# Kernel tuning notes

Measured on AMD Instinct MI355X. Metric: run time of the kernel, lower is better.

Reference implementation:

```python
import jax, jax.numpy as jnp
import numpy as np

LOWERSIZE = 40


def setup_inputs() -> dict:
    key = jax.random.key(0)
    ks = jax.random.split(key, 6)
    N, x_dim, y_dim = 2048, 768, 768
    return {
        "x_samples": jax.random.normal(ks[0], (N, x_dim), dtype=jnp.float32),
        "y_samples": jax.random.normal(ks[1], (N, y_dim), dtype=jnp.float32),
        "W1": jax.random.normal(ks[2], (LOWERSIZE, x_dim + y_dim), dtype=jnp.float32) * 0.02,
        "b1": jax.random.normal(ks[3], (LOWERSIZE,), dtype=jnp.float32) * 0.02,
        "W2": jax.random.normal(ks[4], (1, LOWERSIZE), dtype=jnp.float32) * 0.02,
        "b2": jax.random.normal(ks[5], (1,), dtype=jnp.float32) * 0.02,
    }


def reference(x_samples, y_samples, W1, b1, W2, b2):
    # F(z) = W2 @ relu(W1 @ z + b1) + b2, z = cat(x, y)
    N = y_samples.shape[0]
    x_dim = x_samples.shape[1]
    W1x = W1[:, :x_dim]   # [40, x_dim]
    W1y = W1[:, x_dim:]   # [40, y_dim]

    # Diagonal term T0: F(cat(x_i, y_i)) -> [N, 1]
    h0 = jax.nn.relu(x_samples @ W1x.T + y_samples @ W1y.T + b1)
    T0 = h0 @ W2.T + b2

    # Pairwise term: T1[i, j] = F(cat(x_j, y_i)) - 1.
    # Split the first Linear over x and y to avoid materializing the
    # [N, N, x_dim+y_dim] concatenation (same math, linearity of W1).
    hx = x_samples @ W1x.T  # [N, 40]
    hy = y_samples @ W1y.T  # [N, 40]
    h = jax.nn.relu(hy[:, None, :] + hx[None, :, :] + b1)  # [N, N, 40]
    T1 = (h @ W2.T + b2 - 1.0)[..., 0]  # [N, N]

    lse = jax.nn.logsumexp(T1, axis=1) - jnp.log(jnp.float32(N))  # [N]
    lower_bound = T0.mean() - jnp.exp(lse).mean()
    return lower_bound
```

## Files before the change

kernel.cpp:

```cpp
#include <hip/hip_runtime.h>

#define NROWS 2048
#define KDIM  768
#define L     40
#define HN    (NROWS * L)

__global__ __launch_bounds__(256) void k_proj(const float* __restrict__ x,
                                              const float* __restrict__ y,
                                              const float* __restrict__ W1,
                                              const float* __restrict__ b1,
                                              float* __restrict__ hxb,
                                              float* __restrict__ hy) {
    const int which = blockIdx.y;
    const int oh    = blockIdx.z;
    const float* __restrict__ A = which ? y : x;
    const int tid = threadIdx.x;
    const int r   = tid >> 5;
    const int seg = tid & 31;
    const int row0 = blockIdx.x * 8;

    __shared__ float sh2[8 * 21];

    const float* arow = A + (size_t)(row0 + r) * KDIM;
    float4 a[6];
#pragma unroll
    for (int q = 0; q < 6; ++q)
        a[q] = *(const float4*)(arow + q * 128 + seg * 4);

    const float* wbase = W1 + (size_t)which * KDIM + (size_t)(oh * 20) * (2 * KDIM);
#pragma unroll 2
    for (int ol = 0; ol < 20; ++ol) {
        const float* wrow = wbase + (size_t)ol * (2 * KDIM);
        float s = 0.f;
#pragma unroll
        for (int q = 0; q < 6; ++q) {
            float4 w = *(const float4*)(wrow + q * 128 + seg * 4);
            s += a[q].x * w.x + a[q].y * w.y + a[q].z * w.z + a[q].w * w.w;
        }
        s += __shfl_xor(s, 16);
        s += __shfl_xor(s, 8);
        s += __shfl_xor(s, 4);
        s += __shfl_xor(s, 2);
        s += __shfl_xor(s, 1);
        if (seg == 0) sh2[r * 21 + ol] = s;
    }
    __syncthreads();

    if (tid < 8 * 20) {
        int rr = tid / 20, ol = tid - rr * 20;
        float s = sh2[rr * 21 + ol];
        int o = oh * 20 + ol;
        if (!which) {
            s += b1[o];
            hxb[(size_t)(row0 + rr) * L + o] = s;
        } else {
            hy[(size_t)(row0 + rr) * L + o] = s;
        }
    }
}

#define BI 128
#define BJ 64
#define STRD 44

__global__ __launch_bounds__(512, 4) void k_pair(const float* __restrict__ hxb,
                                                 const float* __restrict__ hy,
                                                 const float* __restrict__ W2,
                                                 const float* __restrict__ b2p,
                                                 float* __restrict__ pairE,
                                                 float* __restrict__ pairT) {
    __shared__ float shy[BI * STRD];
    __shared__ float shx[BJ * STRD];
    __shared__ float sw2[STRD];
    __shared__ float red[16];

    const int tid = threadIdx.x;
    const int i0 = blockIdx.x * BI;
    const int j0 = blockIdx.y * BJ;

    for (int idx = tid; idx < BI * 10; idx += 512) {
        int rr = idx / 10, c = idx - rr * 10;
        float4 v = ((const float4*)(hy + (size_t)i0 * L))[idx];
        *(float4*)(shy + rr * STRD + c * 4) = v;
    }
    for (int idx = tid; idx < BJ * 10; idx += 512) {
        int rr = idx / 10, c = idx - rr * 10;
        float4 v = ((const float4*)(hxb + (size_t)j0 * L))[idx];
        *(float4*)(shx + rr * STRD + c * 4) = v;
    }
    if (tid < 10) ((float4*)sw2)[tid] = ((const float4*)W2)[tid];
    __syncthreads();

    const int tx = tid & 15, ty = tid >> 4;

    float acc[4][4];
#pragma unroll
    for (int u = 0; u < 4; ++u)
#pragma unroll
        for (int v = 0; v < 4; ++v) acc[u][v] = 0.f;

    float4 ayA[4], axA[4], wA4;
    float4 ayB[4], axB[4], wB4;

#define LOADF(AY, AX, W4, K4) do {                                          \
    W4 = *(const float4*)(sw2 + (K4) * 4);                                  \
    _Pragma("unroll") for (int u_ = 0; u_ < 4; ++u_)                        \
        AY[u_] = *(const float4*)(shy + (ty + 32 * u_) * STRD + (K4) * 4);  \
    _Pragma("unroll") for (int v_ = 0; v_ < 4; ++v_)                        \
        AX[v_] = *(const float4*)(shx + (tx + 16 * v_) * STRD + (K4) * 4);  \
} while (0)

#define FMAF(AY, AX, W4) do {                                               \
    _Pragma("unroll") for (int u_ = 0; u_ < 4; ++u_)                        \
    _Pragma("unroll") for (int v_ = 0; v_ < 4; ++v_) {                      \
        float t;                                                            \
        t = AY[u_].x + AX[v_].x; t = fmaxf(t, 0.f); acc[u_][v_] += t * W4.x;\
        t = AY[u_].y + AX[v_].y; t = fmaxf(t, 0.f); acc[u_][v_] += t * W4.y;\
        t = AY[u_].z + AX[v_].z; t = fmaxf(t, 0.f); acc[u_][v_] += t * W4.z;\
        t = AY[u_].w + AX[v_].w; t = fmaxf(t, 0.f); acc[u_][v_] += t * W4.w;\
    }                                                                       \
} while (0)

    LOADF(ayA, axA, wA4, 0);
    LOADF(ayB, axB, wB4, 1);
    FMAF(ayA, axA, wA4); LOADF(ayA, axA, wA4, 2);
    FMAF(ayB, axB, wB4); LOADF(ayB, axB, wB4, 3);
    FMAF(ayA, axA, wA4); LOADF(ayA, axA, wA4, 4);
    FMAF(ayB, axB, wB4); LOADF(ayB, axB, wB4, 5);
    FMAF(ayA, axA, wA4); LOADF(ayA, axA, wA4, 6);
    FMAF(ayB, axB, wB4); LOADF(ayB, axB, wB4, 7);
    FMAF(ayA, axA, wA4); LOADF(ayA, axA, wA4, 8);
    FMAF(ayB, axB, wB4); LOADF(ayB, axB, wB4, 9);
    FMAF(ayA, axA, wA4);
    FMAF(ayB, axB, wB4);

#undef LOADF
#undef FMAF

    const float b2v = b2p[0];
    const float c1  = b2v - 1.f;
    float sumE = 0.f, sumT = 0.f;
#pragma unroll
    for (int u = 0; u < 4; ++u)
#pragma unroll
        for (int v = 0; v < 4; ++v) {
            int gi = i0 + ty + 32 * u;
            int gj = j0 + tx + 16 * v;
            float val = acc[u][v];
            if (gi == gj) sumT += val + b2v;
            sumE += __expf(val + c1);
        }

#pragma unroll
    for (int off = 32; off > 0; off >>= 1) {
        sumE += __shfl_down(sumE, off);
        sumT += __shfl_down(sumT, off);
    }
    int wid = tid >> 6;
    if ((tid & 63) == 0) { red[wid] = sumE; red[8 + wid] = sumT; }
    __syncthreads();
    if (tid == 0) {
        float e = 0.f, t = 0.f;
#pragma unroll
        for (int q = 0; q < 8; ++q) { e += red[q]; t += red[8 + q]; }
        int bid = blockIdx.y * gridDim.x + blockIdx.x;
        pairE[bid] = e;
        pairT[bid] = t;
    }
}

__global__ __launch_bounds__(512) void k_fin(const float* __restrict__ pairE,
                                             const float* __restrict__ pairT,
                                             float* __restrict__ out) {
    __shared__ float red[16];
    const int tid = threadIdx.x;
    float e = pairE[tid];
    float t = pairT[tid];
#pragma unroll
    for (int off = 32; off > 0; off >>= 1) {
        e += __shfl_down(e, off);
        t += __shfl_down(t, off);
    }
    int wid = tid >> 6;
    if ((tid & 63) == 0) { red[wid] = e; red[8 + wid] = t; }
    __syncthreads();
    if (tid == 0) {
        float se = 0.f, st = 0.f;
#pragma unroll
        for (int q = 0; q < 8; ++q) { se += red[q]; st += red[8 + q]; }
        const float invN = 1.0f / (float)NROWS;
        out[0] = st * invN - se * invN * invN;
    }
}

extern "C" void kernel_launch(void* const* d_in, const int* in_sizes, int n_in,
                              void* d_out, int out_size, void* d_ws, size_t ws_size,
                              hipStream_t stream) {
    const float* x  = (const float*)d_in[0];
    const float* y  = (const float*)d_in[1];
    const float* W1 = (const float*)d_in[2];
    const float* b1 = (const float*)d_in[3];
    const float* W2 = (const float*)d_in[4];
    const float* b2 = (const float*)d_in[5];
    float* out = (float*)d_out;

    float* wsf   = (float*)d_ws;
    float* hxb   = wsf;
    float* hy    = hxb + HN;
    float* pairE = hy + HN;
    float* pairT = pairE + 512;

    k_proj<<<dim3(NROWS / 8, 2, 2), 256, 0, stream>>>(x, y, W1, b1, hxb, hy);
    k_pair<<<dim3(NROWS / BI, NROWS / BJ), 512, 0, stream>>>(hxb, hy, W2, b2, pairE, pairT);
    k_fin<<<1, 512, 0, stream>>>(pairE, pairT, out);
}
```

Baseline: 97.15 us.

## Restructure projection kernel to stage W1 slices in LDS with split-K threads

Rewrites k_proj so each block loads a 10-output slice of W1 into shared memory once and reuses it across 32 rows. Each thread handles one row and one 96-float K segment, double-buffering its activation loads, then reduces partial sums through LDS. The aim is to cut repeated global reads of W1 and the per-output wave shuffle reductions of the old design. In exchange, x and y are now read four times (once per output group), and the kernel uses more LDS and registers.

```diff
diff --git a/kernel.cpp b/kernel.cpp
--- a/kernel.cpp
+++ b/kernel.cpp
@@ -4,6 +4,10 @@
 #define KDIM  768
 #define L     40
 #define HN    (NROWS * L)
+
+#define OPB   10
+#define RPB   32
+#define WF4   192
 
 __global__ __launch_bounds__(256) void k_proj(const float* __restrict__ x,
                                               const float* __restrict__ y,
@@ -11,50 +15,73 @@
                                               const float* __restrict__ b1,
                                               float* __restrict__ hxb,
                                               float* __restrict__ hy) {
-    const int which = blockIdx.y;
-    const int oh    = blockIdx.z;
+    const int og    = blockIdx.y;
+    const int which = blockIdx.z;
     const float* __restrict__ A = which ? y : x;
     const int tid = threadIdx.x;
-    const int r   = tid >> 5;
-    const int seg = tid & 31;
-    const int row0 = blockIdx.x * 8;
-
-    __shared__ float sh2[8 * 21];
-
-    const float* arow = A + (size_t)(row0 + r) * KDIM;
-    float4 a[6];
-#pragma unroll
-    for (int q = 0; q < 6; ++q)
-        a[q] = *(const float4*)(arow + q * 128 + seg * 4);
-
-    const float* wbase = W1 + (size_t)which * KDIM + (size_t)(oh * 20) * (2 * KDIM);
-#pragma unroll 2
-    for (int ol = 0; ol < 20; ++ol) {
-        const float* wrow = wbase + (size_t)ol * (2 * KDIM);
-        float s = 0.f;
-#pragma unroll
-        for (int q = 0; q < 6; ++q) {
-            float4 w = *(const float4*)(wrow + q * 128 + seg * 4);
-            s += a[q].x * w.x + a[q].y * w.y + a[q].z * w.z + a[q].w * w.w;
-        }
-        s += __shfl_xor(s, 16);
-        s += __shfl_xor(s, 8);
-        s += __shfl_xor(s, 4);
-        s += __shfl_xor(s, 2);
-        s += __shfl_xor(s, 1);
-        if (seg == 0) sh2[r * 21 + ol] = s;
-    }
-    __syncthreads();
-
-    if (tid < 8 * 20) {
-        int rr = tid / 20, ol = tid - rr * 20;
-        float s = sh2[rr * 21 + ol];
-        int o = oh * 20 + ol;
+    const int r   = tid & 31;
+    const int s   = tid >> 5;
+    const int row0 = blockIdx.x * RPB;
+    const int o0   = og * OPB;
+
+    __shared__ float4 wlds[OPB * WF4];
+
+    const float4* W1f4 = (const float4*)W1;
+    for (int i = tid; i < OPB * WF4; i += 256) {
+        int ol = i / WF4, q = i - ol * WF4;
+        wlds[ol * WF4 + q] = W1f4[(size_t)(o0 + ol) * 384 + which * WF4 + q];
+    }
+
+    const float4* arow = (const float4*)(A + (size_t)(row0 + r) * KDIM) + s * 24;
+
+    float acc[OPB];
+#pragma unroll
+    for (int ol = 0; ol < OPB; ++ol) acc[ol] = 0.f;
+
+    float4 aA[8], aB[8];
+#pragma unroll
+    for (int j = 0; j < 8; ++j) aA[j] = arow[j];
+    __syncthreads();
+
+#define COMPUTE(AR, C) do {                                                  \
+    _Pragma("unroll") for (int ol = 0; ol < OPB; ++ol) {                     \
+        const float4* wp = &wlds[ol * WF4 + s * 24 + (C) * 8];               \
+        float sacc = 0.f;                                                    \
+        _Pragma("unroll") for (int j = 0; j < 8; ++j) {                      \
+            float4 w = wp[j];                                                \
+            sacc += AR[j].x * w.x + AR[j].y * w.y                            \
+                  + AR[j].z * w.z + AR[j].w * w.w;                           \
+        }                                                                    \
+        acc[ol] += sacc;                                                     \
+    } } while (0)
+
+#pragma unroll
+    for (int j = 0; j < 8; ++j) aB[j] = arow[8 + j];
+    COMPUTE(aA, 0);
+#pragma unroll
+    for (int j = 0; j < 8; ++j) aA[j] = arow[16 + j];
+    COMPUTE(aB, 1);
+    COMPUTE(aA, 2);
+#undef COMPUTE
+
+    __syncthreads();
+    float* red = (float*)wlds;
+#pragma unroll
+    for (int ol = 0; ol < OPB; ++ol)
+        red[(ol * 8 + s) * 32 + r] = acc[ol];
+    __syncthreads();
+
+    for (int idx = tid; idx < RPB * OPB; idx += 256) {
+        int rr = idx / OPB, ol = idx - rr * OPB;
+        float v = 0.f;
+#pragma unroll
+        for (int ss = 0; ss < 8; ++ss)
+            v += red[(ol * 8 + ss) * 32 + rr];
+        int o = o0 + ol;
         if (!which) {
-            s += b1[o];
-            hxb[(size_t)(row0 + rr) * L + o] = s;
+            hxb[(size_t)(row0 + rr) * L + o] = v + b1[o];
         } else {
-            hy[(size_t)(row0 + rr) * L + o] = s;
+            hy[(size_t)(row0 + rr) * L + o] = v;
         }
     }
 }
@@ -210,7 +237,7 @@
     float* pairE = hy + HN;
     float* pairT = pairE + 512;
 
-    k_proj<<<dim3(NROWS / 8, 2, 2), 256, 0, stream>>>(x, y, W1, b1, hxb, hy);
+    k_proj<<<dim3(NROWS / RPB, 4, 2), 256, 0, stream>>>(x, y, W1, b1, hxb, hy);
     k_pair<<<dim3(NROWS / BI, NROWS / BJ), 512, 0, stream>>>(hxb, hy, W2, b2, pairE, pairT);
     k_fin<<<1, 512, 0, stream>>>(pairE, pairT, out);
 }
```

Measured after the change: 95.85 us. About the same (-1.3%).

## Fuse projection and pairwise kernels with inter-block flag synchronization

Applied to the files above, without the earlier changes.

Merges the projection kernel into the pairwise kernel. Each of the 512 blocks first computes 4 rows of hx and 4 of hy, then publishes a per-block flag. Blocks spin-wait only on the specific producer blocks whose rows they need before loading tiles. This removes a kernel launch boundary and lets projection and pairwise work overlap, but it depends on all 512 blocks being co-resident to avoid deadlock. The flags use a magic value XOR the block id rather than being reset, so stale flags from an earlier call could satisfy the wait before the data is rewritten.

```diff
diff --git a/kernel.cpp b/kernel.cpp
--- a/kernel.cpp
+++ b/kernel.cpp
@@ -4,79 +4,78 @@
 #define KDIM  768
 #define L     40
 #define HN    (NROWS * L)
-
-__global__ __launch_bounds__(256) void k_proj(const float* __restrict__ x,
-                                              const float* __restrict__ y,
-                                              const float* __restrict__ W1,
-                                              const float* __restrict__ b1,
-                                              float* __restrict__ hxb,
-                                              float* __restrict__ hy) {
-    const int which = blockIdx.y;
-    const int oh    = blockIdx.z;
-    const float* __restrict__ A = which ? y : x;
-    const int tid = threadIdx.x;
-    const int r   = tid >> 5;
-    const int seg = tid & 31;
-    const int row0 = blockIdx.x * 8;
-
-    __shared__ float sh2[8 * 21];
-
-    const float* arow = A + (size_t)(row0 + r) * KDIM;
-    float4 a[6];
-#pragma unroll
-    for (int q = 0; q < 6; ++q)
-        a[q] = *(const float4*)(arow + q * 128 + seg * 4);
-
-    const float* wbase = W1 + (size_t)which * KDIM + (size_t)(oh * 20) * (2 * KDIM);
-#pragma unroll 2
-    for (int ol = 0; ol < 20; ++ol) {
-        const float* wrow = wbase + (size_t)ol * (2 * KDIM);
-        float s = 0.f;
-#pragma unroll
-        for (int q = 0; q < 6; ++q) {
-            float4 w = *(const float4*)(wrow + q * 128 + seg * 4);
-            s += a[q].x * w.x + a[q].y * w.y + a[q].z * w.z + a[q].w * w.w;
-        }
-        s += __shfl_xor(s, 16);
-        s += __shfl_xor(s, 8);
-        s += __shfl_xor(s, 4);
-        s += __shfl_xor(s, 2);
-        s += __shfl_xor(s, 1);
-        if (seg == 0) sh2[r * 21 + ol] = s;
-    }
-    __syncthreads();
-
-    if (tid < 8 * 20) {
-        int rr = tid / 20, ol = tid - rr * 20;
-        float s = sh2[rr * 21 + ol];
-        int o = oh * 20 + ol;
-        if (!which) {
-            s += b1[o];
-            hxb[(size_t)(row0 + rr) * L + o] = s;
-        } else {
-            hy[(size_t)(row0 + rr) * L + o] = s;
-        }
-    }
-}
+#define MAGICF 0x7A3F0000u
 
 #define BI 128
 #define BJ 64
 #define STRD 44
 
-__global__ __launch_bounds__(512, 4) void k_pair(const float* __restrict__ hxb,
-                                                 const float* __restrict__ hy,
-                                                 const float* __restrict__ W2,
-                                                 const float* __restrict__ b2p,
-                                                 float* __restrict__ pairE,
-                                                 float* __restrict__ pairT) {
+__global__ __launch_bounds__(512, 4) void k_fused(
+    const float* __restrict__ x, const float* __restrict__ y,
+    const float* __restrict__ W1, const float* __restrict__ b1,
+    const float* __restrict__ W2, const float* __restrict__ b2p,
+    float* __restrict__ hxb, float* __restrict__ hy,
+    unsigned* __restrict__ flags,
+    float* __restrict__ pairE, float* __restrict__ pairT)
+{
+    const int tid  = threadIdx.x;
+    const int b    = blockIdx.x;
+    const int wv   = tid >> 6;
+    const int lane = tid & 63;
+
+    {
+        const int which = wv >> 2;
+        const int row   = b * 4 + (wv & 3);
+        const float* A  = which ? y : x;
+        const float4* af = (const float4*)(A + (size_t)row * KDIM);
+        float4 a0 = af[lane], a1 = af[64 + lane], a2 = af[128 + lane];
+        const float4* wb = (const float4*)W1 + which * 192;
+        float keep = 0.f;
+#pragma unroll 4
+        for (int o = 0; o < L; ++o) {
+            const float4* wf = wb + (size_t)o * 384;
+            float4 w0 = wf[lane], w1 = wf[64 + lane], w2 = wf[128 + lane];
+            float s = a0.x*w0.x + a0.y*w0.y + a0.z*w0.z + a0.w*w0.w
+                    + a1.x*w1.x + a1.y*w1.y + a1.z*w1.z + a1.w*w1.w
+                    + a2.x*w2.x + a2.y*w2.y + a2.z*w2.z + a2.w*w2.w;
+            s += __shfl_xor(s, 32);
+            s += __shfl_xor(s, 16);
+            s += __shfl_xor(s, 8);
+            s += __shfl_xor(s, 4);
+            s += __shfl_xor(s, 2);
+            s += __shfl_xor(s, 1);
+            if (lane == o) keep = s;
+        }
+        if (lane < L) {
+            float v = keep;
+            if (!which) { v += b1[lane]; hxb[(size_t)row * L + lane] = v; }
+            else        {                hy [(size_t)row * L + lane] = v; }
+        }
+    }
+    __syncthreads();
+    if (tid == 0) {
+        __threadfence();
+        __hip_atomic_store(&flags[b], MAGICF ^ (unsigned)b,
+                           __ATOMIC_RELEASE, __HIP_MEMORY_SCOPE_AGENT);
+    }
+
+    const int bx = b & 15, by = b >> 4;
+    const int i0 = bx * BI, j0 = by * BJ;
+
+    if (tid < 48) {
+        int p = (tid < 32) ? (bx * 32 + tid) : (by * 16 + (tid - 32));
+        unsigned want = MAGICF ^ (unsigned)p;
+        while (__hip_atomic_load(&flags[p], __ATOMIC_RELAXED,
+                                 __HIP_MEMORY_SCOPE_AGENT) != want)
+            __builtin_amdgcn_s_sleep(2);
+        __threadfence();
+    }
+    __syncthreads();
+
     __shared__ float shy[BI * STRD];
     __shared__ float shx[BJ * STRD];
     __shared__ float sw2[STRD];
     __shared__ float red[16];
-
-    const int tid = threadIdx.x;
-    const int i0 = blockIdx.x * BI;
-    const int j0 = blockIdx.y * BJ;
 
     for (int idx = tid; idx < BI * 10; idx += 512) {
         int rr = idx / 10, c = idx - rr * 10;
@@ -163,9 +162,8 @@
         float e = 0.f, t = 0.f;
 #pragma unroll
         for (int q = 0; q < 8; ++q) { e += red[q]; t += red[8 + q]; }
-        int bid = blockIdx.y * gridDim.x + blockIdx.x;
-        pairE[bid] = e;
-        pairT[bid] = t;
+        pairE[b] = e;
+        pairT[b] = t;
     }
 }
 
@@ -204,13 +202,14 @@
     const float* b2 = (const float*)d_in[5];
     float* out = (float*)d_out;
 
-    float* wsf   = (float*)d_ws;
-    float* hxb   = wsf;
-    float* hy    = hxb + HN;
-    float* pairE = hy + HN;
-    float* pairT = pairE + 512;
-
-    k_proj<<<dim3(NROWS / 8, 2, 2), 256, 0, stream>>>(x, y, W1, b1, hxb, hy);
-    k_pair<<<dim3(NROWS / BI, NROWS / BJ), 512, 0, stream>>>(hxb, hy, W2, b2, pairE, pairT);
+    float* wsf      = (float*)d_ws;
+    unsigned* flags = (unsigned*)wsf;
+    float* hxb      = wsf + 512;
+    float* hy       = hxb + HN;
+    float* pairE    = hy + HN;
+    float* pairT    = pairE + 512;
+
+    k_fused<<<512, 512, 0, stream>>>(x, y, W1, b1, W2, b2,
+                                     hxb, hy, flags, pairE, pairT);
     k_fin<<<1, 512, 0, stream>>>(pairE, pairT, out);
 }
```

Measured after the change: 129.2 us. +33.0%, slower.
